# Kernel optimization log

Measured on AMD Instinct MI355X. Metric: run time of the kernel, lower is better.

The kernel has to match this reference:

```python
import jax, jax.numpy as jnp
import numpy as np

EPS = 1e-5  # torch GroupNorm default eps

def setup_inputs() -> dict:
    key = jax.random.key(0)
    ks = jax.random.split(key, 6)
    B, H, W, C = 16, 64, 64, 768
    T, R = 8, 64
    x = jax.random.normal(ks[0], (B, H, W, C), dtype=jnp.float32)
    task_ids = jax.random.randint(ks[1], (B,), 0, T, dtype=jnp.int32)
    gamma = jnp.ones((C,), dtype=jnp.float32)
    beta = jnp.zeros((C,), dtype=jnp.float32)
    # kaiming-uniform-ish scale for down proj; up proj small (zeros in torch init,
    # but use small random so gradients are non-trivial)
    W_down = jax.random.normal(ks[2], (T, R, C), dtype=jnp.float32) / jnp.sqrt(jnp.float32(C))
    W_up = jax.random.normal(ks[3], (T, C, R), dtype=jnp.float32) * 0.02
    scales = jnp.ones((T,), dtype=jnp.float32)
    return {"x": x, "task_ids": task_ids, "gamma": gamma, "beta": beta,
            "W_down": W_down, "W_up": W_up, "scales": scales}

def reference(x, task_ids, gamma, beta, W_down, W_up, scales):
    # GroupNorm(num_groups=1): normalize each sample over (H, W, C), per-channel affine
    mean = jnp.mean(x, axis=(1, 2, 3), keepdims=True)
    var = jnp.var(x, axis=(1, 2, 3), keepdims=True)
    x_norm = (x - mean) * jax.lax.rsqrt(var + EPS) * gamma + beta  # [B,H,W,C]
    # Gather per-sample expert weights (1x1 convs == low-rank linear maps)
    Wd = W_down[task_ids]          # [B, R, C]
    Wu = W_up[task_ids]            # [B, C, R]
    s = scales[task_ids]           # [B]
    h = jnp.einsum('bhwc,brc->bhwr', x_norm, Wd)
    h = jax.nn.gelu(h, approximate=False)  # torch nn.GELU default is exact erf
    delta = jnp.einsum('bhwr,bcr->bhwc', h, Wu)
    return x + s[:, None, None, None] * delta
```

## Files before the change

### kernel.cpp

```cpp
#include <hip/hip_runtime.h>
#include <hip/hip_bf16.h>

#define BATCH 16
#define C 768
#define T 8
#define R 64
#define HW 4096
#define NPS (HW*C)
#define GN_EPS 1e-5f
#define NPART 48

typedef short bf16x8 __attribute__((ext_vector_type(8)));
typedef float f32x4 __attribute__((ext_vector_type(4)));

static __device__ __forceinline__ unsigned short f2bf(float f) {
    __hip_bfloat16 h = __float2bfloat16(f);
    return *reinterpret_cast<unsigned short*>(&h);
}

__global__ __launch_bounds__(256) void prep_stats_kernel(
        const float* __restrict__ Wdn, const float* __restrict__ Wup,
        const float* __restrict__ gamma, const float* __restrict__ beta,
        const float* __restrict__ x,
        float* __restrict__ partials,
        unsigned short* __restrict__ wdg, unsigned short* __restrict__ wu_bf,
        float* __restrict__ u, float* __restrict__ w) {
    int bid = blockIdx.x;
    int tid = threadIdx.x;
    if (bid < 768) {
        int idx = bid * 256 + tid;
        const int NF4 = T * R * C / 4;
        if (idx < NF4) {
            int c4 = idx % (C / 4);
            float4 v = ((const float4*)Wdn)[idx];
            float4 g = ((const float4*)gamma)[c4];
            ushort4 o;
            o.x = f2bf(v.x * g.x); o.y = f2bf(v.y * g.y);
            o.z = f2bf(v.z * g.z); o.w = f2bf(v.w * g.w);
            *reinterpret_cast<ushort4*>(wdg + idx * 4) = o;
        } else {
            int j = idx - NF4;
            float4 v = ((const float4*)Wup)[j];
            ushort4 o;
            o.x = f2bf(v.x); o.y = f2bf(v.y); o.z = f2bf(v.z); o.w = f2bf(v.w);
            *reinterpret_cast<ushort4*>(wu_bf + j * 4) = o;
        }
    } else if (bid < 896) {
        int rowid = (bid - 768) * 4 + (tid >> 6);
        int lane = tid & 63;
        const float* wrow = Wdn + (size_t)rowid * C;
        float su = 0.f, sw = 0.f;
        #pragma unroll
        for (int j = 0; j < 12; j++) {
            int c = lane + j * 64;
            float wv = wrow[c];
            su += wv * gamma[c];
            sw += wv * beta[c];
        }
        for (int off = 32; off > 0; off >>= 1) {
            su += __shfl_down(su, off);
            sw += __shfl_down(sw, off);
        }
        if (lane == 0) { u[rowid] = su; w[rowid] = sw; }
    } else {
        int sblk = bid - 896;
        int b = sblk / NPART, part = sblk % NPART;
        const float4* xp = (const float4*)(x + (size_t)b * NPS);
        float s = 0.f, q = 0.f;
        int base = part * 256 + tid;
        #pragma unroll 4
        for (int i = 0; i < 64; i++) {
            float4 v = xp[(size_t)i * 12288 + base];
            s += v.x + v.y + v.z + v.w;
            q += v.x*v.x + v.y*v.y + v.z*v.z + v.w*v.w;
        }
        for (int off = 32; off > 0; off >>= 1) {
            s += __shfl_down(s, off);
            q += __shfl_down(q, off);
        }
        __shared__ float ps[4], pq[4];
        int wave = tid >> 6, lane = tid & 63;
        if (lane == 0) { ps[wave] = s; pq[wave] = q; }
        __syncthreads();
        if (tid == 0) {
            float S = 0.f, Q = 0.f;
            #pragma unroll
            for (int wv = 0; wv < 4; wv++) { S += ps[wv]; Q += pq[wv]; }
            partials[(b * NPART + part) * 2]     = S;
            partials[(b * NPART + part) * 2 + 1] = Q;
        }
    }
}

__global__ __launch_bounds__(256, 1) void fused_kernel(
        const float* __restrict__ x, const int* __restrict__ task_ids,
        const float* __restrict__ scales, const float* __restrict__ partials,
        const unsigned short* __restrict__ wdg, const unsigned short* __restrict__ wu_bf,
        const float* __restrict__ u, const float* __restrict__ w,
        float* __restrict__ out) {
    __shared__ char xsb[3 * 49152];
    __shared__ char hsb[2048];

    int bid = blockIdx.x;
    int b = bid >> 4;
    int chunk = bid & 15;
    int tid = threadIdx.x;
    int wv = tid >> 6, lane = tid & 63;
    int lr = lane & 15, lg = lane >> 4;
    int swz = (lr & 7) << 4;

    int t = task_ids[b];
    float sc = scales[t];

    float s1 = 0.f, s2 = 0.f;
    if (lane < NPART) {
        float2 v = ((const float2*)(partials + b * 2 * NPART))[lane];
        s1 = v.x; s2 = v.y;
    }
    #pragma unroll
    for (int off = 32; off > 0; off >>= 1) {
        s1 += __shfl_xor(s1, off);
        s2 += __shfl_xor(s2, off);
    }
    float mean = s1 * (1.f / NPS);
    float var  = s2 * (1.f / NPS) - mean * mean;
    float rstd = rsqrtf(var + GN_EPS);

    const unsigned short* wdp = wdg + t * (R * C);
    bf16x8 a1[24];
    #pragma unroll
    for (int k = 0; k < 24; k++)
        a1[k] = *reinterpret_cast<const bf16x8*>(wdp + (wv * 16 + lr) * C + k * 32 + lg * 8);
    const unsigned short* wup = wu_bf + t * (C * R);
    bf16x8 a2[12][2];
    #pragma unroll
    for (int cb = 0; cb < 12; cb++)
        #pragma unroll
        for (int ks = 0; ks < 2; ks++)
            a2[cb][ks] = *reinterpret_cast<const bf16x8*>(
                wup + (wv * 192 + cb * 16 + lr) * R + ks * 32 + lg * 8);

    int r0 = wv * 16 + lg * 4;
    float4 u4 = *reinterpret_cast<const float4*>(u + t * 64 + r0);
    float4 w4 = *reinterpret_cast<const float4*>(w + t * 64 + r0);
    float mb = rstd * mean;
    float bias0 = w4.x - mb * u4.x, bias1 = w4.y - mb * u4.y;
    float bias2 = w4.z - mb * u4.z, bias3 = w4.w - mb * u4.w;

    size_t base = (size_t)b * NPS + (size_t)chunk * 256 * C;
    const char* xbase_c = (const char*)(x + base);
    float* outp = out + base;
    const char* hcb = hsb;

#define STAGE(ldbuf, tileidx) do {                                               \
    const char* _gs = xbase_c + (size_t)(tileidx) * 49152;                       \
    char* _ld = (ldbuf);                                                         \
    _Pragma("unroll")                                                            \
    for (int _jj = 0; _jj < 12; _jj++) {                                         \
        int _j = wv * 12 + _jj;                                                  \
        int _row = _j / 3;                                                       \
        int _sub = _j - _row * 3;                                                \
        int _cb = (_sub * 1024 + lane * 16) ^ ((_row & 7) << 4);                 \
        __builtin_amdgcn_global_load_lds(                                        \
            (const __attribute__((address_space(1))) void*)(_gs + _row * 3072 + _cb), \
            (__attribute__((address_space(3))) void*)(_ld + (size_t)_j * 1024),  \
            16, 0, 0);                                                           \
    }                                                                            \
} while (0)

    char* bufA = xsb;
    char* bufB = xsb + 49152;
    char* bufC = xsb + 98304;

    STAGE(bufA, 0);
    STAGE(bufB, 1);

    for (int i = 0; i < 16; i++) {
        if (i == 0 || i == 15) asm volatile("s_waitcnt vmcnt(12)" ::: "memory");
        else                   asm volatile("s_waitcnt vmcnt(24)" ::: "memory");
        __builtin_amdgcn_s_barrier();
        if (i + 2 < 16) STAGE(bufC, i + 2);

        const char* xb = bufA;

        f32x4 acc1 = {0.f, 0.f, 0.f, 0.f};
        #pragma unroll
        for (int k = 0; k < 24; k++) {
            int cb0 = (k * 128 + lg * 32) ^ swz;
            int cb1 = (k * 128 + lg * 32 + 16) ^ swz;
            f32x4 xv0 = *reinterpret_cast<const f32x4*>(xb + lr * 3072 + cb0);
            f32x4 xv1 = *reinterpret_cast<const f32x4*>(xb + lr * 3072 + cb1);
            bf16x8 bfrag;
            bfrag[0] = (short)f2bf(xv0[0]); bfrag[1] = (short)f2bf(xv0[1]);
            bfrag[2] = (short)f2bf(xv0[2]); bfrag[3] = (short)f2bf(xv0[3]);
            bfrag[4] = (short)f2bf(xv1[0]); bfrag[5] = (short)f2bf(xv1[1]);
            bfrag[6] = (short)f2bf(xv1[2]); bfrag[7] = (short)f2bf(xv1[3]);
            acc1 = __builtin_amdgcn_mfma_f32_16x16x32_bf16(a1[k], bfrag, acc1, 0, 0, 0);
        }

        {
            float v0 = rstd * acc1[0] + bias0;
            float v1 = rstd * acc1[1] + bias1;
            float v2 = rstd * acc1[2] + bias2;
            float v3 = rstd * acc1[3] + bias3;
            ushort4 o;
            o.x = f2bf(0.5f * v0 * (1.f + erff(v0 * 0.70710678118f)));
            o.y = f2bf(0.5f * v1 * (1.f + erff(v1 * 0.70710678118f)));
            o.z = f2bf(0.5f * v2 * (1.f + erff(v2 * 0.70710678118f)));
            o.w = f2bf(0.5f * v3 * (1.f + erff(v3 * 0.70710678118f)));
            int byte = lr * 128 + ((wv * 32 + lg * 8) ^ swz);
            *reinterpret_cast<ushort4*>(hsb + byte) = o;
        }
        asm volatile("s_waitcnt lgkmcnt(0)" ::: "memory");
        __builtin_amdgcn_s_barrier();

        bf16x8 b2[2];
        #pragma unroll
        for (int ks = 0; ks < 2; ks++) {
            int byte = lr * 128 + ((ks * 64 + lg * 16) ^ swz);
            b2[ks] = *reinterpret_cast<const bf16x8*>(hcb + byte);
        }
        size_t ro = (size_t)(i * 16 + lr) * C;
        #pragma unroll
        for (int cb = 0; cb < 12; cb++) {
            f32x4 acc = {0.f, 0.f, 0.f, 0.f};
            acc = __builtin_amdgcn_mfma_f32_16x16x32_bf16(a2[cb][0], b2[0], acc, 0, 0, 0);
            acc = __builtin_amdgcn_mfma_f32_16x16x32_bf16(a2[cb][1], b2[1], acc, 0, 0, 0);
            int c0 = wv * 192 + cb * 16 + lg * 4;
            float4 xr = *reinterpret_cast<const float4*>(xb + lr * 3072 + ((c0 * 4) ^ swz));
            float4 ov;
            ov.x = xr.x + sc * acc[0];
            ov.y = xr.y + sc * acc[1];
            ov.z = xr.z + sc * acc[2];
            ov.w = xr.w + sc * acc[3];
            *reinterpret_cast<float4*>(outp + ro + c0) = ov;
        }

        char* tmp = bufA; bufA = bufB; bufB = bufC; bufC = tmp;
    }
#undef STAGE
}

extern "C" void kernel_launch(void* const* d_in, const int* in_sizes, int n_in,
                              void* d_out, int out_size, void* d_ws, size_t ws_size,
                              hipStream_t stream) {
    const float* x        = (const float*)d_in[0];
    const int*   task_ids = (const int*)d_in[1];
    const float* gamma    = (const float*)d_in[2];
    const float* beta     = (const float*)d_in[3];
    const float* W_down   = (const float*)d_in[4];
    const float* W_up     = (const float*)d_in[5];
    const float* scales   = (const float*)d_in[6];
    float* out = (float*)d_out;

    float* partials = (float*)d_ws;
    unsigned short* wdg   = (unsigned short*)((char*)d_ws + 8192);
    unsigned short* wu_bf = wdg + T * R * C;
    float* u = (float*)((char*)d_ws + 8192 + 2 * T * R * C * sizeof(unsigned short));
    float* w = u + T * R;

    prep_stats_kernel<<<1664, 256, 0, stream>>>(W_down, W_up, gamma, beta, x,
                                                partials, wdg, wu_bf, u, w);
    fused_kernel<<<256, 256, 0, stream>>>(x, task_ids, scales, partials,
                                          wdg, wu_bf, u, w, out);
}
```

Before: 120.7 us.

## Warp-specialize fused kernel into producer and consumer wave groups

Doubles the block to 512 threads and splits the waves into two roles. Four waves load x tiles and compute the down-projection plus GELU. The other four waves run the up-projection and residual store one tile behind, with a double-buffered h in shared memory. The goal is to overlap the two GEMM stages and spread the register-held weights across more waves. The risks are barrier-count mismatches between the two roles, and a possible race on the triple-buffered x tiles: the producer can overwrite a buffer while the consumer is still reading it for the residual.

Result: faster. 116.8 us (-3.2%).

```diff
diff --git a/kernel.cpp b/kernel.cpp
--- a/kernel.cpp
+++ b/kernel.cpp
@@ -92,20 +92,20 @@
     }
 }
 
-__global__ __launch_bounds__(256, 1) void fused_kernel(
+__global__ __launch_bounds__(512, 1) void fused_kernel(
         const float* __restrict__ x, const int* __restrict__ task_ids,
         const float* __restrict__ scales, const float* __restrict__ partials,
         const unsigned short* __restrict__ wdg, const unsigned short* __restrict__ wu_bf,
         const float* __restrict__ u, const float* __restrict__ w,
         float* __restrict__ out) {
     __shared__ char xsb[3 * 49152];
-    __shared__ char hsb[2048];
+    __shared__ char hsb[2][2048];
 
     int bid = blockIdx.x;
     int b = bid >> 4;
     int chunk = bid & 15;
     int tid = threadIdx.x;
-    int wv = tid >> 6, lane = tid & 63;
+    int wvid = tid >> 6, lane = tid & 63;
     int lr = lane & 15, lg = lane >> 4;
     int swz = (lr & 7) << 4;
 
@@ -126,38 +126,16 @@
     float var  = s2 * (1.f / NPS) - mean * mean;
     float rstd = rsqrtf(var + GN_EPS);
 
-    const unsigned short* wdp = wdg + t * (R * C);
-    bf16x8 a1[24];
-    #pragma unroll
-    for (int k = 0; k < 24; k++)
-        a1[k] = *reinterpret_cast<const bf16x8*>(wdp + (wv * 16 + lr) * C + k * 32 + lg * 8);
-    const unsigned short* wup = wu_bf + t * (C * R);
-    bf16x8 a2[12][2];
-    #pragma unroll
-    for (int cb = 0; cb < 12; cb++)
-        #pragma unroll
-        for (int ks = 0; ks < 2; ks++)
-            a2[cb][ks] = *reinterpret_cast<const bf16x8*>(
-                wup + (wv * 192 + cb * 16 + lr) * R + ks * 32 + lg * 8);
-
-    int r0 = wv * 16 + lg * 4;
-    float4 u4 = *reinterpret_cast<const float4*>(u + t * 64 + r0);
-    float4 w4 = *reinterpret_cast<const float4*>(w + t * 64 + r0);
-    float mb = rstd * mean;
-    float bias0 = w4.x - mb * u4.x, bias1 = w4.y - mb * u4.y;
-    float bias2 = w4.z - mb * u4.z, bias3 = w4.w - mb * u4.w;
-
     size_t base = (size_t)b * NPS + (size_t)chunk * 256 * C;
     const char* xbase_c = (const char*)(x + base);
     float* outp = out + base;
-    const char* hcb = hsb;
 
 #define STAGE(ldbuf, tileidx) do {                                               \
     const char* _gs = xbase_c + (size_t)(tileidx) * 49152;                       \
     char* _ld = (ldbuf);                                                         \
     _Pragma("unroll")                                                            \
     for (int _jj = 0; _jj < 12; _jj++) {                                         \
-        int _j = wv * 12 + _jj;                                                  \
+        int _j = pw * 12 + _jj;                                                  \
         int _row = _j / 3;                                                       \
         int _sub = _j - _row * 3;                                                \
         int _cb = (_sub * 1024 + lane * 16) ^ ((_row & 7) << 4);                 \
@@ -168,75 +146,131 @@
     }                                                                            \
 } while (0)
 
-    char* bufA = xsb;
-    char* bufB = xsb + 49152;
-    char* bufC = xsb + 98304;
-
-    STAGE(bufA, 0);
-    STAGE(bufB, 1);
-
-    for (int i = 0; i < 16; i++) {
-        if (i == 0 || i == 15) asm volatile("s_waitcnt vmcnt(12)" ::: "memory");
-        else                   asm volatile("s_waitcnt vmcnt(24)" ::: "memory");
-        __builtin_amdgcn_s_barrier();
-        if (i + 2 < 16) STAGE(bufC, i + 2);
-
-        const char* xb = bufA;
-
-        f32x4 acc1 = {0.f, 0.f, 0.f, 0.f};
+    if (wvid < 4) {
+        int pw = wvid;
+        const unsigned short* wdp = wdg + t * (R * C);
+        bf16x8 a1[24];
         #pragma unroll
-        for (int k = 0; k < 24; k++) {
-            int cb0 = (k * 128 + lg * 32) ^ swz;
-            int cb1 = (k * 128 + lg * 32 + 16) ^ swz;
-            f32x4 xv0 = *reinterpret_cast<const f32x4*>(xb + lr * 3072 + cb0);
-            f32x4 xv1 = *reinterpret_cast<const f32x4*>(xb + lr * 3072 + cb1);
-            bf16x8 bfrag;
-            bfrag[0] = (short)f2bf(xv0[0]); bfrag[1] = (short)f2bf(xv0[1]);
-            bfrag[2] = (short)f2bf(xv0[2]); bfrag[3] = (short)f2bf(xv0[3]);
-            bfrag[4] = (short)f2bf(xv1[0]); bfrag[5] = (short)f2bf(xv1[1]);
-            bfrag[6] = (short)f2bf(xv1[2]); bfrag[7] = (short)f2bf(xv1[3]);
-            acc1 = __builtin_amdgcn_mfma_f32_16x16x32_bf16(a1[k], bfrag, acc1, 0, 0, 0);
-        }
-
-        {
-            float v0 = rstd * acc1[0] + bias0;
-            float v1 = rstd * acc1[1] + bias1;
-            float v2 = rstd * acc1[2] + bias2;
-            float v3 = rstd * acc1[3] + bias3;
+        for (int k = 0; k < 24; k++)
+            a1[k] = *reinterpret_cast<const bf16x8*>(wdp + (pw * 16 + lr) * C + k * 32 + lg * 8);
+
+        int r0 = pw * 16 + lg * 4;
+        float4 u4 = *reinterpret_cast<const float4*>(u + t * 64 + r0);
+        float4 w4 = *reinterpret_cast<const float4*>(w + t * 64 + r0);
+        float mb = rstd * mean;
+        float bias0 = w4.x - mb * u4.x, bias1 = w4.y - mb * u4.y;
+        float bias2 = w4.z - mb * u4.z, bias3 = w4.w - mb * u4.w;
+
+        STAGE(xsb, 0);
+        STAGE(xsb + 49152, 1);
+
+        for (int i = 0; i < 16; i++) {
+            if (i == 15) asm volatile("s_waitcnt vmcnt(0)" ::: "memory");
+            else         asm volatile("s_waitcnt vmcnt(12)" ::: "memory");
+
+            const char* xb = xsb + (i % 3) * 49152;
+            f32x4 acc1a = {0.f, 0.f, 0.f, 0.f};
+            f32x4 acc1b = {0.f, 0.f, 0.f, 0.f};
+            #pragma unroll
+            for (int k = 0; k < 24; k += 2) {
+                #pragma unroll
+                for (int kk = 0; kk < 2; kk++) {
+                    int kc = k + kk;
+                    int cb0 = (kc * 128 + lg * 32) ^ swz;
+                    int cb1 = (kc * 128 + lg * 32 + 16) ^ swz;
+                    f32x4 xv0 = *reinterpret_cast<const f32x4*>(xb + lr * 3072 + cb0);
+                    f32x4 xv1 = *reinterpret_cast<const f32x4*>(xb + lr * 3072 + cb1);
+                    bf16x8 bfrag;
+                    bfrag[0] = (short)f2bf(xv0[0]); bfrag[1] = (short)f2bf(xv0[1]);
+                    bfrag[2] = (short)f2bf(xv0[2]); bfrag[3] = (short)f2bf(xv0[3]);
+                    bfrag[4] = (short)f2bf(xv1[0]); bfrag[5] = (short)f2bf(xv1[1]);
+                    bfrag[6] = (short)f2bf(xv1[2]); bfrag[7] = (short)f2bf(xv1[3]);
+                    if (kk == 0)
+                        acc1a = __builtin_amdgcn_mfma_f32_16x16x32_bf16(a1[kc], bfrag, acc1a, 0, 0, 0);
+                    else
+                        acc1b = __builtin_amdgcn_mfma_f32_16x16x32_bf16(a1[kc], bfrag, acc1b, 0, 0, 0);
+                }
+            }
+            float v0 = rstd * (acc1a[0] + acc1b[0]) + bias0;
+            float v1 = rstd * (acc1a[1] + acc1b[1]) + bias1;
+            float v2 = rstd * (acc1a[2] + acc1b[2]) + bias2;
+            float v3 = rstd * (acc1a[3] + acc1b[3]) + bias3;
             ushort4 o;
             o.x = f2bf(0.5f * v0 * (1.f + erff(v0 * 0.70710678118f)));
             o.y = f2bf(0.5f * v1 * (1.f + erff(v1 * 0.70710678118f)));
             o.z = f2bf(0.5f * v2 * (1.f + erff(v2 * 0.70710678118f)));
             o.w = f2bf(0.5f * v3 * (1.f + erff(v3 * 0.70710678118f)));
-            int byte = lr * 128 + ((wv * 32 + lg * 8) ^ swz);
-            *reinterpret_cast<ushort4*>(hsb + byte) = o;
-        }
-        asm volatile("s_waitcnt lgkmcnt(0)" ::: "memory");
-        __builtin_amdgcn_s_barrier();
-
-        bf16x8 b2[2];
+            int hbyte = lr * 128 + ((pw * 32 + lg * 8) ^ swz);
+            *reinterpret_cast<ushort4*>(hsb[i & 1] + hbyte) = o;
+
+            asm volatile("s_waitcnt lgkmcnt(0)" ::: "memory");
+            __builtin_amdgcn_s_barrier();
+            if (i + 2 < 16) STAGE(xsb + ((i + 2) % 3) * 49152, i + 2);
+        }
+    } else {
+        int cw = wvid - 4;
+        const unsigned short* wup = wu_bf + t * (C * R);
+        bf16x8 a2[12][2];
         #pragma unroll
-        for (int ks = 0; ks < 2; ks++) {
-            int byte = lr * 128 + ((ks * 64 + lg * 16) ^ swz);
-            b2[ks] = *reinterpret_cast<const bf16x8*>(hcb + byte);
-        }
-        size_t ro = (size_t)(i * 16 + lr) * C;
-        #pragma unroll
-        for (int cb = 0; cb < 12; cb++) {
-            f32x4 acc = {0.f, 0.f, 0.f, 0.f};
-            acc = __builtin_amdgcn_mfma_f32_16x16x32_bf16(a2[cb][0], b2[0], acc, 0, 0, 0);
-            acc = __builtin_amdgcn_mfma_f32_16x16x32_bf16(a2[cb][1], b2[1], acc, 0, 0, 0);
-            int c0 = wv * 192 + cb * 16 + lg * 4;
-            float4 xr = *reinterpret_cast<const float4*>(xb + lr * 3072 + ((c0 * 4) ^ swz));
-            float4 ov;
-            ov.x = xr.x + sc * acc[0];
-            ov.y = xr.y + sc * acc[1];
-            ov.z = xr.z + sc * acc[2];
-            ov.w = xr.w + sc * acc[3];
-            *reinterpret_cast<float4*>(outp + ro + c0) = ov;
-        }
-
-        char* tmp = bufA; bufA = bufB; bufB = bufC; bufC = tmp;
+        for (int cb = 0; cb < 12; cb++)
+            #pragma unroll
+            for (int ks = 0; ks < 2; ks++)
+                a2[cb][ks] = *reinterpret_cast<const bf16x8*>(
+                    wup + (cw * 192 + cb * 16 + lr) * R + ks * 32 + lg * 8);
+
+        for (int i = 0; i < 16; i++) {
+            if (i > 0) {
+                int j = i - 1;
+                const char* xb = xsb + (j % 3) * 49152;
+                bf16x8 b2[2];
+                #pragma unroll
+                for (int ks = 0; ks < 2; ks++) {
+                    int byte = lr * 128 + ((ks * 64 + lg * 16) ^ swz);
+                    b2[ks] = *reinterpret_cast<const bf16x8*>(hsb[j & 1] + byte);
+                }
+                size_t ro = (size_t)(j * 16 + lr) * C;
+                #pragma unroll
+                for (int cb = 0; cb < 12; cb++) {
+                    f32x4 acc = {0.f, 0.f, 0.f, 0.f};
+                    acc = __builtin_amdgcn_mfma_f32_16x16x32_bf16(a2[cb][0], b2[0], acc, 0, 0, 0);
+                    acc = __builtin_amdgcn_mfma_f32_16x16x32_bf16(a2[cb][1], b2[1], acc, 0, 0, 0);
+                    int c0 = cw * 192 + cb * 16 + lg * 4;
+                    float4 xr = *reinterpret_cast<const float4*>(xb + lr * 3072 + ((c0 * 4) ^ swz));
+                    float4 ov;
+                    ov.x = xr.x + sc * acc[0];
+                    ov.y = xr.y + sc * acc[1];
+                    ov.z = xr.z + sc * acc[2];
+                    ov.w = xr.w + sc * acc[3];
+                    *reinterpret_cast<float4*>(outp + ro + c0) = ov;
+                }
+            }
+            __builtin_amdgcn_s_barrier();
+        }
+        {
+            int j = 15;
+            const char* xb = xsb + (j % 3) * 49152;
+            bf16x8 b2[2];
+            #pragma unroll
+            for (int ks = 0; ks < 2; ks++) {
+                int byte = lr * 128 + ((ks * 64 + lg * 16) ^ swz);
+                b2[ks] = *reinterpret_cast<const bf16x8*>(hsb[j & 1] + byte);
+            }
+            size_t ro = (size_t)(j * 16 + lr) * C;
+            #pragma unroll
+            for (int cb = 0; cb < 12; cb++) {
+                f32x4 acc = {0.f, 0.f, 0.f, 0.f};
+                acc = __builtin_amdgcn_mfma_f32_16x16x32_bf16(a2[cb][0], b2[0], acc, 0, 0, 0);
+                acc = __builtin_amdgcn_mfma_f32_16x16x32_bf16(a2[cb][1], b2[1], acc, 0, 0, 0);
+                int c0 = cw * 192 + cb * 16 + lg * 4;
+                float4 xr = *reinterpret_cast<const float4*>(xb + lr * 3072 + ((c0 * 4) ^ swz));
+                float4 ov;
+                ov.x = xr.x + sc * acc[0];
+                ov.y = xr.y + sc * acc[1];
+                ov.z = xr.z + sc * acc[2];
+                ov.w = xr.w + sc * acc[3];
+                *reinterpret_cast<float4*>(outp + ro + c0) = ov;
+            }
+        }
     }
 #undef STAGE
 }
@@ -261,6 +295,6 @@
 
     prep_stats_kernel<<<1664, 256, 0, stream>>>(W_down, W_up, gamma, beta, x,
                                                 partials, wdg, wu_bf, u, w);
-    fused_kernel<<<256, 256, 0, stream>>>(x, task_ids, scales, partials,
+    fused_kernel<<<256, 512, 0, stream>>>(x, task_ids, scales, partials,
                                           wdg, wu_bf, u, w, out);
 }
```

## Add warp-specialized fused kernel reading a bf16 copy of x from the stats pass

Applied to the files above, without the earlier changes.

The stats pre-pass now also writes a bf16 copy of x into the workspace. A new 512-thread fused kernel splits its waves into producers and consumers. Producer waves stage bf16 x tiles into LDS and compute the down-projection plus GELU. Consumer waves compute the up-projection and write the residual output, double-buffering h through LDS. The old path, used when the workspace is too small, gets two independent MFMA accumulators to break the dependency chain. Total DRAM traffic stays about the same, and the residual now uses bf16-rounded x, which costs accuracy.

After: 144.6 us. 19.8% more time.

```diff
diff --git a/kernel.cpp b/kernel.cpp
--- a/kernel.cpp
+++ b/kernel.cpp
@@ -8,7 +8,6 @@
 #define HW 4096
 #define NPS (HW*C)
 #define GN_EPS 1e-5f
-#define NPART 48
 
 typedef short bf16x8 __attribute__((ext_vector_type(8)));
 typedef float f32x4 __attribute__((ext_vector_type(4)));
@@ -17,7 +16,261 @@
     __hip_bfloat16 h = __float2bfloat16(f);
     return *reinterpret_cast<unsigned short*>(&h);
 }
-
+static __device__ __forceinline__ float bf2f(unsigned short u) {
+    return __uint_as_float(((unsigned)u) << 16);
+}
+
+
+__global__ __launch_bounds__(256) void prepA(
+        const float* __restrict__ Wdn, const float* __restrict__ Wup,
+        const float* __restrict__ gamma, const float* __restrict__ beta,
+        const float* __restrict__ x,
+        float* __restrict__ partials,
+        unsigned short* __restrict__ wdg, unsigned short* __restrict__ wu_bf,
+        float* __restrict__ u, float* __restrict__ w,
+        unsigned short* __restrict__ xw) {
+    int bid = blockIdx.x;
+    int tid = threadIdx.x;
+    if (bid < 768) {
+        int idx = bid * 256 + tid;
+        const int NF4 = T * R * C / 4;
+        if (idx < NF4) {
+            int c4 = idx % (C / 4);
+            float4 v = ((const float4*)Wdn)[idx];
+            float4 g = ((const float4*)gamma)[c4];
+            ushort4 o;
+            o.x = f2bf(v.x * g.x); o.y = f2bf(v.y * g.y);
+            o.z = f2bf(v.z * g.z); o.w = f2bf(v.w * g.w);
+            *reinterpret_cast<ushort4*>(wdg + idx * 4) = o;
+        } else {
+            int j = idx - NF4;
+            float4 v = ((const float4*)Wup)[j];
+            ushort4 o;
+            o.x = f2bf(v.x); o.y = f2bf(v.y); o.z = f2bf(v.z); o.w = f2bf(v.w);
+            *reinterpret_cast<ushort4*>(wu_bf + j * 4) = o;
+        }
+    } else if (bid < 896) {
+        int rowid = (bid - 768) * 4 + (tid >> 6);
+        int lane = tid & 63;
+        const float* wrow = Wdn + (size_t)rowid * C;
+        float su = 0.f, sw = 0.f;
+        #pragma unroll
+        for (int j = 0; j < 12; j++) {
+            int c = lane + j * 64;
+            float wv = wrow[c];
+            su += wv * gamma[c];
+            sw += wv * beta[c];
+        }
+        for (int off = 32; off > 0; off >>= 1) {
+            su += __shfl_down(su, off);
+            sw += __shfl_down(sw, off);
+        }
+        if (lane == 0) { u[rowid] = su; w[rowid] = sw; }
+    } else {
+        int sblk = bid - 896;
+        int b = sblk >> 6, part = sblk & 63;
+        const float4* xp = (const float4*)(x + (size_t)b * NPS);
+        ushort4* xw4 = (ushort4*)(xw + (size_t)b * NPS);
+        int base = part * 12288;
+        float s = 0.f, q = 0.f;
+        #pragma unroll 4
+        for (int j = 0; j < 24; j++) {
+            int idx = base + j * 512 + 2 * tid;
+            float4 v0 = xp[idx], v1 = xp[idx + 1];
+            s += v0.x + v0.y + v0.z + v0.w + v1.x + v1.y + v1.z + v1.w;
+            q += v0.x*v0.x + v0.y*v0.y + v0.z*v0.z + v0.w*v0.w
+               + v1.x*v1.x + v1.y*v1.y + v1.z*v1.z + v1.w*v1.w;
+            ushort4 o0, o1;
+            o0.x = f2bf(v0.x); o0.y = f2bf(v0.y); o0.z = f2bf(v0.z); o0.w = f2bf(v0.w);
+            o1.x = f2bf(v1.x); o1.y = f2bf(v1.y); o1.z = f2bf(v1.z); o1.w = f2bf(v1.w);
+            xw4[idx] = o0;
+            xw4[idx + 1] = o1;
+        }
+        for (int off = 32; off > 0; off >>= 1) {
+            s += __shfl_down(s, off);
+            q += __shfl_down(q, off);
+        }
+        __shared__ float ps[4], pq[4];
+        int wave = tid >> 6, lane = tid & 63;
+        if (lane == 0) { ps[wave] = s; pq[wave] = q; }
+        __syncthreads();
+        if (tid == 0) {
+            float S = 0.f, Q = 0.f;
+            #pragma unroll
+            for (int wv = 0; wv < 4; wv++) { S += ps[wv]; Q += pq[wv]; }
+            partials[(b * 64 + part) * 2]     = S;
+            partials[(b * 64 + part) * 2 + 1] = Q;
+        }
+    }
+}
+
+__global__ __launch_bounds__(512, 2) void fusedB(
+        const int* __restrict__ task_ids, const float* __restrict__ scales,
+        const float* __restrict__ partials,
+        const unsigned short* __restrict__ wdg, const unsigned short* __restrict__ wu_bf,
+        const float* __restrict__ u, const float* __restrict__ w,
+        const unsigned short* __restrict__ xw, float* __restrict__ out) {
+    __shared__ char xsb[3 * 49152];
+    __shared__ char hsb[2][4096];
+
+    int bid = blockIdx.x;
+    int b = bid >> 4;
+    int chunk = bid & 15;
+    int tid = threadIdx.x;
+    int wvid = tid >> 6, lane = tid & 63;
+    int lr = lane & 15, lg = lane >> 4;
+    int swz = (lr & 7) << 4;
+
+    int t = task_ids[b];
+    float sc = scales[t];
+
+    float2 pv = ((const float2*)partials)[b * 64 + lane];
+    float s1 = pv.x, s2 = pv.y;
+    #pragma unroll
+    for (int off = 32; off > 0; off >>= 1) {
+        s1 += __shfl_xor(s1, off);
+        s2 += __shfl_xor(s2, off);
+    }
+    float mean = s1 * (1.f / NPS);
+    float var  = s2 * (1.f / NPS) - mean * mean;
+    float rstd = rsqrtf(var + GN_EPS);
+    float mb = rstd * mean;
+
+    size_t basee = (size_t)b * NPS + (size_t)chunk * 256 * C;
+    const char* xwbase = (const char*)(xw + basee);
+    float* outp = out + basee;
+
+    if (wvid < 4) {
+        int pw = wvid;
+
+        const unsigned short* wdp = wdg + t * (R * C) + (size_t)(pw * 16 + lr) * C;
+        bf16x8 a1[24];
+        #pragma unroll
+        for (int k = 0; k < 24; k++)
+            a1[k] = *reinterpret_cast<const bf16x8*>(wdp + k * 32 + lg * 8);
+
+        int r0 = pw * 16 + lg * 4;
+        float4 u4 = *reinterpret_cast<const float4*>(u + t * 64 + r0);
+        float4 w4 = *reinterpret_cast<const float4*>(w + t * 64 + r0);
+        float bias0 = w4.x - mb * u4.x, bias1 = w4.y - mb * u4.y;
+        float bias2 = w4.z - mb * u4.z, bias3 = w4.w - mb * u4.w;
+
+        int soff[12];
+        #pragma unroll
+        for (int jj = 0; jj < 12; jj++) {
+            int j = pw * 12 + jj;
+            int dstb = j * 1024 + lane * 16;
+            int row = dstb / 1536;
+            int col = dstb - row * 1536;
+            soff[jj] = row * 1536 + (col ^ ((row & 7) << 4));
+        }
+
+#define STAGE(bufsel, ti) do {                                                   \
+    const char* _gs = xwbase + (size_t)(ti) * 49152;                             \
+    char* _ld = xsb + (bufsel) * 49152;                                          \
+    _Pragma("unroll")                                                            \
+    for (int _jj = 0; _jj < 12; _jj++) {                                         \
+        __builtin_amdgcn_global_load_lds(                                        \
+            (const __attribute__((address_space(1))) void*)(_gs + soff[_jj]),    \
+            (__attribute__((address_space(3))) void*)(_ld + (pw * 12 + _jj) * 1024), \
+            16, 0, 0);                                                           \
+    }                                                                            \
+} while (0)
+
+        STAGE(0, 0);
+        STAGE(1, 1);
+
+        for (int i = 0; i < 8; i++) {
+            if (i == 7) asm volatile("s_waitcnt vmcnt(0)" ::: "memory");
+            else        asm volatile("s_waitcnt vmcnt(12)" ::: "memory");
+            __builtin_amdgcn_s_barrier();
+
+            const char* xb = xsb + (i % 3) * 49152;
+            f32x4 acc[2] = {};
+            #pragma unroll
+            for (int k = 0; k < 24; k++) {
+                #pragma unroll
+                for (int xh = 0; xh < 2; xh++) {
+                    int rowl = xh * 16 + lr;
+                    bf16x8 bfrag = *reinterpret_cast<const bf16x8*>(
+                        xb + rowl * 1536 + ((k * 64 + lg * 16) ^ swz));
+                    acc[xh] = __builtin_amdgcn_mfma_f32_16x16x32_bf16(a1[k], bfrag, acc[xh], 0, 0, 0);
+                }
+            }
+            #pragma unroll
+            for (int xh = 0; xh < 2; xh++) {
+                float v0 = rstd * acc[xh][0] + bias0;
+                float v1 = rstd * acc[xh][1] + bias1;
+                float v2 = rstd * acc[xh][2] + bias2;
+                float v3 = rstd * acc[xh][3] + bias3;
+                ushort4 o;
+                o.x = f2bf(0.5f * v0 * (1.f + erff(v0 * 0.70710678118f)));
+                o.y = f2bf(0.5f * v1 * (1.f + erff(v1 * 0.70710678118f)));
+                o.z = f2bf(0.5f * v2 * (1.f + erff(v2 * 0.70710678118f)));
+                o.w = f2bf(0.5f * v3 * (1.f + erff(v3 * 0.70710678118f)));
+                int hbyte = (xh * 16 + lr) * 128 + ((pw * 32 + lg * 8) ^ swz);
+                *reinterpret_cast<ushort4*>(hsb[i & 1] + hbyte) = o;
+            }
+            asm volatile("s_waitcnt lgkmcnt(0)" ::: "memory");
+            __builtin_amdgcn_s_barrier();
+            if (i + 2 < 8) STAGE((i + 2) % 3, i + 2);
+        }
+#undef STAGE
+    } else {
+        int cw = wvid - 4;
+
+        const unsigned short* wup = wu_bf + t * (C * R);
+        bf16x8 a2[12][2];
+        #pragma unroll
+        for (int cb = 0; cb < 12; cb++)
+            #pragma unroll
+            for (int ks = 0; ks < 2; ks++)
+                a2[cb][ks] = *reinterpret_cast<const bf16x8*>(
+                    wup + (size_t)(cw * 192 + cb * 16 + lr) * R + ks * 32 + lg * 8);
+
+        #define CONSUME(jj) do {                                                     \
+            int j_ = (jj);                                                           \
+            const char* xb = xsb + (j_ % 3) * 49152;                                 \
+            const char* hb = hsb[j_ & 1];                                            \
+            bf16x8 b2[2][2];                                                         \
+            _Pragma("unroll")                                                        \
+            for (int xh = 0; xh < 2; xh++)                                           \
+                _Pragma("unroll")                                                    \
+                for (int ks = 0; ks < 2; ks++)                                       \
+                    b2[xh][ks] = *reinterpret_cast<const bf16x8*>(                   \
+                        hb + (xh * 16 + lr) * 128 + ((ks * 64 + lg * 16) ^ swz));    \
+            _Pragma("unroll")                                                        \
+            for (int cb = 0; cb < 12; cb++) {                                        \
+                int c0 = cw * 192 + cb * 16 + lg * 4;                                \
+                _Pragma("unroll")                                                    \
+                for (int xh = 0; xh < 2; xh++) {                                     \
+                    f32x4 acc = {0.f, 0.f, 0.f, 0.f};                                \
+                    acc = __builtin_amdgcn_mfma_f32_16x16x32_bf16(a2[cb][0], b2[xh][0], acc, 0, 0, 0); \
+                    acc = __builtin_amdgcn_mfma_f32_16x16x32_bf16(a2[cb][1], b2[xh][1], acc, 0, 0, 0); \
+                    int rowl = xh * 16 + lr;                                         \
+                    ushort4 rv = *reinterpret_cast<const ushort4*>(                  \
+                        xb + rowl * 1536 + ((c0 * 2) ^ swz));                        \
+                    float4 ov;                                                       \
+                    ov.x = bf2f(rv.x) + sc * acc[0];                                 \
+                    ov.y = bf2f(rv.y) + sc * acc[1];                                 \
+                    ov.z = bf2f(rv.z) + sc * acc[2];                                 \
+                    ov.w = bf2f(rv.w) + sc * acc[3];                                 \
+                    *reinterpret_cast<float4*>(outp + (size_t)(j_ * 32 + rowl) * C + c0) = ov; \
+                }                                                                    \
+            }                                                                        \
+        } while (0)
+
+        for (int i = 0; i < 8; i++) {
+            __builtin_amdgcn_s_barrier();
+            if (i > 0) CONSUME(i - 1);
+            __builtin_amdgcn_s_barrier();
+        }
+        CONSUME(7);
+        #undef CONSUME
+    }
+}
+
+#define NPART 48
 __global__ __launch_bounds__(256) void prep_stats_kernel(
         const float* __restrict__ Wdn, const float* __restrict__ Wup,
         const float* __restrict__ gamma, const float* __restrict__ beta,
@@ -182,35 +435,40 @@
         if (i + 2 < 16) STAGE(bufC, i + 2);
 
         const char* xb = bufA;
-
-        f32x4 acc1 = {0.f, 0.f, 0.f, 0.f};
-        #pragma unroll
-        for (int k = 0; k < 24; k++) {
-            int cb0 = (k * 128 + lg * 32) ^ swz;
-            int cb1 = (k * 128 + lg * 32 + 16) ^ swz;
-            f32x4 xv0 = *reinterpret_cast<const f32x4*>(xb + lr * 3072 + cb0);
-            f32x4 xv1 = *reinterpret_cast<const f32x4*>(xb + lr * 3072 + cb1);
-            bf16x8 bfrag;
-            bfrag[0] = (short)f2bf(xv0[0]); bfrag[1] = (short)f2bf(xv0[1]);
-            bfrag[2] = (short)f2bf(xv0[2]); bfrag[3] = (short)f2bf(xv0[3]);
-            bfrag[4] = (short)f2bf(xv1[0]); bfrag[5] = (short)f2bf(xv1[1]);
-            bfrag[6] = (short)f2bf(xv1[2]); bfrag[7] = (short)f2bf(xv1[3]);
-            acc1 = __builtin_amdgcn_mfma_f32_16x16x32_bf16(a1[k], bfrag, acc1, 0, 0, 0);
-        }
-
-        {
-            float v0 = rstd * acc1[0] + bias0;
-            float v1 = rstd * acc1[1] + bias1;
-            float v2 = rstd * acc1[2] + bias2;
-            float v3 = rstd * acc1[3] + bias3;
-            ushort4 o;
-            o.x = f2bf(0.5f * v0 * (1.f + erff(v0 * 0.70710678118f)));
-            o.y = f2bf(0.5f * v1 * (1.f + erff(v1 * 0.70710678118f)));
-            o.z = f2bf(0.5f * v2 * (1.f + erff(v2 * 0.70710678118f)));
-            o.w = f2bf(0.5f * v3 * (1.f + erff(v3 * 0.70710678118f)));
-            int byte = lr * 128 + ((wv * 32 + lg * 8) ^ swz);
-            *reinterpret_cast<ushort4*>(hsb + byte) = o;
-        }
+        f32x4 acc1a = {0.f, 0.f, 0.f, 0.f};
+        f32x4 acc1b = {0.f, 0.f, 0.f, 0.f};
+        #pragma unroll
+        for (int k = 0; k < 24; k += 2) {
+            #pragma unroll
+            for (int kk = 0; kk < 2; kk++) {
+                int kc = k + kk;
+                int cb0 = (kc * 128 + lg * 32) ^ swz;
+                int cb1 = (kc * 128 + lg * 32 + 16) ^ swz;
+                f32x4 xv0 = *reinterpret_cast<const f32x4*>(xb + lr * 3072 + cb0);
+                f32x4 xv1 = *reinterpret_cast<const f32x4*>(xb + lr * 3072 + cb1);
+                bf16x8 bfrag;
+                bfrag[0] = (short)f2bf(xv0[0]); bfrag[1] = (short)f2bf(xv0[1]);
+                bfrag[2] = (short)f2bf(xv0[2]); bfrag[3] = (short)f2bf(xv0[3]);
+                bfrag[4] = (short)f2bf(xv1[0]); bfrag[5] = (short)f2bf(xv1[1]);
+                bfrag[6] = (short)f2bf(xv1[2]); bfrag[7] = (short)f2bf(xv1[3]);
+                if (kk == 0)
+                    acc1a = __builtin_amdgcn_mfma_f32_16x16x32_bf16(a1[kc], bfrag, acc1a, 0, 0, 0);
+                else
+                    acc1b = __builtin_amdgcn_mfma_f32_16x16x32_bf16(a1[kc], bfrag, acc1b, 0, 0, 0);
+            }
+        }
+        float v0 = rstd * (acc1a[0] + acc1b[0]) + bias0;
+        float v1 = rstd * (acc1a[1] + acc1b[1]) + bias1;
+        float v2 = rstd * (acc1a[2] + acc1b[2]) + bias2;
+        float v3 = rstd * (acc1a[3] + acc1b[3]) + bias3;
+        ushort4 o;
+        o.x = f2bf(0.5f * v0 * (1.f + erff(v0 * 0.70710678118f)));
+        o.y = f2bf(0.5f * v1 * (1.f + erff(v1 * 0.70710678118f)));
+        o.z = f2bf(0.5f * v2 * (1.f + erff(v2 * 0.70710678118f)));
+        o.w = f2bf(0.5f * v3 * (1.f + erff(v3 * 0.70710678118f)));
+        int hbyte = lr * 128 + ((wv * 32 + lg * 8) ^ swz);
+        *reinterpret_cast<ushort4*>(hsb + hbyte) = o;
+
         asm volatile("s_waitcnt lgkmcnt(0)" ::: "memory");
         __builtin_amdgcn_s_barrier();
 
@@ -253,14 +511,37 @@
     const float* scales   = (const float*)d_in[6];
     float* out = (float*)d_out;
 
-    float* partials = (float*)d_ws;
-    unsigned short* wdg   = (unsigned short*)((char*)d_ws + 8192);
-    unsigned short* wu_bf = wdg + T * R * C;
-    float* u = (float*)((char*)d_ws + 8192 + 2 * T * R * C * sizeof(unsigned short));
-    float* w = u + T * R;
-
-    prep_stats_kernel<<<1664, 256, 0, stream>>>(W_down, W_up, gamma, beta, x,
-                                                partials, wdg, wu_bf, u, w);
-    fused_kernel<<<256, 256, 0, stream>>>(x, task_ids, scales, partials,
-                                          wdg, wu_bf, u, w, out);
-}
+    const size_t OFF_PART = 0;
+    const size_t OFF_WDG  = 16384;
+    const size_t OFF_WU   = OFF_WDG + 786432;
+    const size_t OFF_U    = OFF_WU + 786432;
+    const size_t OFF_W    = OFF_U + 2048;
+    const size_t OFF_XW   = 1593344;
+    const size_t XW_BYTES = (size_t)BATCH * NPS * 2;
+    const size_t NEED     = OFF_XW + XW_BYTES;
+
+    if (ws_size >= NEED) {
+        float* partials       = (float*)((char*)d_ws + OFF_PART);
+        unsigned short* wdg   = (unsigned short*)((char*)d_ws + OFF_WDG);
+        unsigned short* wu_bf = (unsigned short*)((char*)d_ws + OFF_WU);
+        float* u              = (float*)((char*)d_ws + OFF_U);
+        float* w              = (float*)((char*)d_ws + OFF_W);
+        unsigned short* xw    = (unsigned short*)((char*)d_ws + OFF_XW);
+
+        prepA<<<1920, 256, 0, stream>>>(W_down, W_up, gamma, beta, x,
+                                        partials, wdg, wu_bf, u, w, xw);
+        fusedB<<<256, 512, 0, stream>>>(task_ids, scales, partials,
+                                        wdg, wu_bf, u, w, xw, out);
+    } else {
+        float* partials       = (float*)d_ws;
+        unsigned short* wdg   = (unsigned short*)((char*)d_ws + 8192);
+        unsigned short* wu_bf = wdg + T * R * C;
+        float* u = (float*)((char*)d_ws + 8192 + 2 * T * R * C * sizeof(unsigned short));
+        float* w = u + T * R;
+
+        prep_stats_kernel<<<1664, 256, 0, stream>>>(W_down, W_up, gamma, beta, x,
+                                                    partials, wdg, wu_bf, u, w);
+        fused_kernel<<<256, 256, 0, stream>>>(x, task_ids, scales, partials,
+                                              wdg, wu_bf, u, w, out);
+    }
+}
```
